# Kernel tuning notes

Measured on AMD Instinct MI355X. Metric: run time of the kernel, lower is better.

The kernel has to match this reference:

```python
import jax, jax.numpy as jnp
import numpy as np

N_NODES = 100000
N_EDGES = 1600000


def _lin_init(k, din, dout):
    # xavier-normal-ish weight, zero bias handled separately
    s = (2.0 / (din + dout)) ** 0.5
    return jax.random.normal(k, (din, dout), jnp.float32) * s


def setup_inputs() -> dict:
    key = jax.random.key(0)
    ks = jax.random.split(key, 32)
    inp = {
        "node_feat": jax.random.normal(ks[0], (N_NODES, 3), jnp.float32),
        "edge_feat": jax.random.normal(ks[1], (N_EDGES, 1), jnp.float32),
        "edge_dist": jax.random.normal(ks[2], (N_EDGES, 1), jnp.float32),
        "src": jax.random.randint(ks[3], (N_EDGES,), 0, N_NODES),
        "dst": jax.random.randint(ks[4], (N_EDGES,), 0, N_NODES),
    }
    dims = {"enc": [3, 64, 64, 8], "dec": [8, 64, 64, 1],
            "nod": [9, 64, 64, 8], "edg": [17, 64, 64, 1]}
    i = 5
    for name, d in dims.items():
        for l in range(3):
            inp[f"w_{name}{l+1}"] = _lin_init(ks[i], d[l], d[l + 1]); i += 1
            inp[f"b_{name}{l+1}"] = jnp.zeros((d[l + 1],), jnp.float32)
    return inp


def _mlp(x, w1, b1, w2, b2, w3, b3):
    x = jax.nn.relu(x @ w1 + b1)
    x = jax.nn.relu(x @ w2 + b2)
    return jax.nn.relu(x @ w3 + b3)


def _edge_softmax(dist, dst, n):
    # softmax over incoming edges per destination node (DGL edge_softmax)
    m = jax.ops.segment_max(dist, dst, num_segments=n)          # [N,1]
    e = jnp.exp(dist - m[dst])                                   # [E,1]
    s = jax.ops.segment_sum(e, dst, num_segments=n)              # [N,1]
    return e / s[dst]


def reference(node_feat, edge_feat, edge_dist, src, dst,
              w_enc1, b_enc1, w_enc2, b_enc2, w_enc3, b_enc3,
              w_dec1, b_dec1, w_dec2, b_dec2, w_dec3, b_dec3,
              w_nod1, b_nod1, w_nod2, b_nod2, w_nod3, b_nod3,
              w_edg1, b_edg1, w_edg2, b_edg2, w_edg3, b_edg3):
    n = node_feat.shape[0]
    # encoder: [N,3] -> [N,8]
    h = _mlp(node_feat, w_enc1, b_enc1, w_enc2, b_enc2, w_enc3, b_enc3)
    # softmax-weighted aggregation of src features to dst
    w = _edge_softmax(edge_dist, dst, n)                         # [E,1]
    h = jax.ops.segment_sum(w * h[src], dst, num_segments=n)     # [N,8]
    he = edge_feat                                               # [E,1]
    for _ in range(2):
        x = jnp.concatenate([he, h[src], h[dst]], axis=-1)       # [E,17]
        he = _mlp(x, w_edg1, b_edg1, w_edg2, b_edg2, w_edg3, b_edg3)  # [E,1]
        agg = jax.ops.segment_sum(he, dst, num_segments=n)       # [N,1]
        h = _mlp(jnp.concatenate([agg, h], axis=-1),
                 w_nod1, b_nod1, w_nod2, b_nod2, w_nod3, b_nod3)  # [N,8]
    # second softmax aggregation (same dist -> same weights)
    h = jax.ops.segment_sum(w * h[src], dst, num_segments=n)     # [N,8]
    # decoder: [N,8] -> [N,1]
    return _mlp(h, w_dec1, b_dec1, w_dec2, b_dec2, w_dec3, b_dec3)
```

## Files before the change

kernel.cpp:

```cpp
#include <hip/hip_runtime.h>
#include <hip/hip_bf16.h>

#define N_NODES 100000
#define N_EDGES 1600000

typedef __attribute__((ext_vector_type(4))) float f32x4;
typedef __attribute__((ext_vector_type(8))) short bf16x8;

__device__ __forceinline__ unsigned short f2bf(float v) {
    return __builtin_bit_cast(unsigned short, __float2bfloat16(v));
}
__device__ __forceinline__ float bf2f(unsigned short h) {
    return __uint_as_float(((unsigned)h) << 16);
}

__global__ void zero_kernel(float* p, int n) {
    int i = blockIdx.x * blockDim.x + threadIdx.x;
    int stride = gridDim.x * blockDim.x;
    for (; i < n; i += stride) p[i] = 0.f;
}

__global__ void exp_agg_kernel(const float* __restrict__ dist,
                               const int* __restrict__ src, const int* __restrict__ dst,
                               const float* __restrict__ h,
                               float* __restrict__ s, float* __restrict__ wbuf,
                               float* __restrict__ hagg, int E) {
    int t = blockIdx.x * blockDim.x + threadIdx.x;
    if (t >= E * 8) return;
    int e = t >> 3, c = t & 7;
    float v = expf(dist[e]);
    int d = dst[e];
    if (c == 0) {
        wbuf[e] = v;
        atomicAdd(s + d, v);
    }
    atomicAdd(hagg + d * 8 + c, v * h[src[e] * 8 + c]);
}

__global__ void agg2_kernel(const float* __restrict__ wbuf, const float* __restrict__ h,
                            const int* __restrict__ src, const int* __restrict__ dst,
                            float* __restrict__ out, int E) {
    int t = blockIdx.x * blockDim.x + threadIdx.x;
    if (t >= E * 8) return;
    int e = t >> 3, c = t & 7;
    float v = wbuf[e];
    atomicAdd(out + dst[e] * 8 + c, v * h[src[e] * 8 + c]);
}

__global__ void norm_kernel(float* __restrict__ hagg, const float* __restrict__ s,
                            float* __restrict__ rs, int N) {
    int d = blockIdx.x * blockDim.x + threadIdx.x;
    if (d >= N) return;
    float r = 1.f / s[d];
    rs[d] = r;
    float4 a = *(const float4*)(hagg + d * 8);
    float4 b = *(const float4*)(hagg + d * 8 + 4);
    a.x *= r; a.y *= r; a.z *= r; a.w *= r;
    b.x *= r; b.y *= r; b.z *= r; b.w *= r;
    *(float4*)(hagg + d * 8) = a;
    *(float4*)(hagg + d * 8 + 4) = b;
}

struct PackArgs { const float *w1, *b1, *w2; float* out; int din, stride; };

__global__ void pack_kernel(PackArgs a0, PackArgs a1, PackArgs a2) {
    PackArgs a = (blockIdx.x == 0) ? a0 : (blockIdx.x == 1) ? a1 : a2;
    int k = threadIdx.x;
    float* row = a.out + k * a.stride;
    for (int j = 0; j < 64; ++j) row[j] = a.w2[k * 64 + j];
    for (int j = 0; j < a.din; ++j) row[64 + j] = a.w1[j * 64 + k];
    row[64 + a.din] = a.b1[k];
}

__global__ void pack_edge_kernel(const float* __restrict__ w1, const float* __restrict__ w2,
                                 unsigned short* __restrict__ w1hi, unsigned short* __restrict__ w1lo,
                                 unsigned short* __restrict__ w2hi, unsigned short* __restrict__ w2lo) {
    int c = threadIdx.x;
    for (int j = 0; j < 32; ++j) {
        float v = (j < 17) ? w1[j * 64 + c] : 0.f;
        unsigned short hi = f2bf(v);
        w1hi[c * 32 + j] = hi;
        w1lo[c * 32 + j] = f2bf(v - bf2f(hi));
    }
    int mt = c >> 4, row = c & 15;
    for (int ch = 0; ch < 64; ++ch) {
        int ks = ch >> 5, r5 = ch & 31;
        int i = ((r5 >> 4) << 2) | (r5 & 3);
        int g = (r5 >> 2) & 3;
        int dstIdx = (((mt * 2 + ks) * 16 + row) * 4 + g) * 8 + i;
        float v = w2[ch * 64 + c];
        unsigned short hi = f2bf(v);
        w2hi[dstIdx] = hi;
        w2lo[dstIdx] = f2bf(v - bf2f(hi));
    }
}

template <int DIN, int DOUT, int STRIDE>
__device__ __forceinline__ void mlp_fused(
    const float* __restrict__ x, const float* __restrict__ wp,
    const float* __restrict__ b2,
    const float* __restrict__ w3, const float* __restrict__ b3,
    float* __restrict__ out) {
    float h2[64];
#pragma unroll
    for (int j = 0; j < 64; ++j) h2[j] = b2[j];
    for (int k = 0; k < 64; ++k) {
        const float* row = wp + k * STRIDE;
        float a = row[64 + DIN];
#pragma unroll
        for (int j = 0; j < DIN; ++j) a = fmaf(x[j], row[64 + j], a);
        a = fmaxf(a, 0.f);
#pragma unroll
        for (int j = 0; j < 64; ++j) h2[j] = fmaf(a, row[j], h2[j]);
    }
    float acc[DOUT];
#pragma unroll
    for (int o = 0; o < DOUT; ++o) acc[o] = b3[o];
#pragma unroll
    for (int j = 0; j < 64; ++j) {
        float r = fmaxf(h2[j], 0.f);
#pragma unroll
        for (int o = 0; o < DOUT; ++o) acc[o] = fmaf(r, w3[j * DOUT + o], acc[o]);
    }
#pragma unroll
    for (int o = 0; o < DOUT; ++o) out[o] = fmaxf(acc[o], 0.f);
}

template <int CA, int CB, int DOUT, int STRIDE>
__global__ __launch_bounds__(256, 3) void node_mlp_kernel(
    const float* __restrict__ xa, const float* __restrict__ xb,
    const float* __restrict__ rs,
    const float* __restrict__ wp, const float* __restrict__ b2,
    const float* __restrict__ w3, const float* __restrict__ b3,
    float* __restrict__ out, int n) {
    constexpr int DIN = CA + CB;
    int i = blockIdx.x * 256 + threadIdx.x;
    if (i >= n) return;
    float scale = rs ? rs[i] : 1.f;
    float x[DIN];
#pragma unroll
    for (int k = 0; k < CA; ++k) x[k] = xa[i * CA + k] * scale;
    if (CB == 8) {
        float4 v0 = *(const float4*)(xb + i * 8);
        float4 v1 = *(const float4*)(xb + i * 8 + 4);
        x[CA + 0] = v0.x; x[CA + 1] = v0.y; x[CA + 2] = v0.z; x[CA + 3] = v0.w;
        x[CA + 4] = v1.x; x[CA + 5] = v1.y; x[CA + 6] = v1.z; x[CA + 7] = v1.w;
    }
    float o[DOUT];
    mlp_fused<DIN, DOUT, STRIDE>(x, wp, b2, w3, b3, o);
#pragma unroll
    for (int k = 0; k < DOUT; ++k) out[i * DOUT + k] = o[k];
}

__global__ __launch_bounds__(128, 2) void edge_mlp_mfma_kernel(
    const float* __restrict__ he_in, const float* __restrict__ h,
    const int* __restrict__ src, const int* __restrict__ dst,
    const unsigned short* __restrict__ w1hi, const unsigned short* __restrict__ w1lo,
    const unsigned short* __restrict__ w2hi, const unsigned short* __restrict__ w2lo,
    const float* __restrict__ b1, const float* __restrict__ b2,
    const float* __restrict__ w3, const float* __restrict__ b3,
    float* __restrict__ he_out, float* __restrict__ agg) {
    __shared__ __align__(16) unsigned char smem[2 * 10240];
    const int lane = threadIdx.x & 63, wv = threadIdx.x >> 6;
    unsigned char* W = smem + wv * 10240;
    const int ebase = (blockIdx.x * 2 + wv) * 64;

    {
        int e = ebase + lane;
        float x[32];
        x[0] = he_in[e];
        int sr = src[e], dd = dst[e];
        float4 a0 = *(const float4*)(h + sr * 8);
        float4 a1 = *(const float4*)(h + sr * 8 + 4);
        float4 d0 = *(const float4*)(h + dd * 8);
        float4 d1 = *(const float4*)(h + dd * 8 + 4);
        x[1] = a0.x;  x[2] = a0.y;  x[3] = a0.z;  x[4] = a0.w;
        x[5] = a1.x;  x[6] = a1.y;  x[7] = a1.z;  x[8] = a1.w;
        x[9] = d0.x;  x[10] = d0.y; x[11] = d0.z; x[12] = d0.w;
        x[13] = d1.x; x[14] = d1.y; x[15] = d1.z; x[16] = d1.w;
#pragma unroll
        for (int j = 17; j < 32; ++j) x[j] = 0.f;
        unsigned uh[16], ul[16];
#pragma unroll
        for (int jj = 0; jj < 16; ++jj) {
            unsigned short h0 = f2bf(x[2 * jj]);
            unsigned short h1v = f2bf(x[2 * jj + 1]);
            unsigned short l0 = f2bf(x[2 * jj] - bf2f(h0));
            unsigned short l1 = f2bf(x[2 * jj + 1] - bf2f(h1v));
            uh[jj] = (unsigned)h0 | ((unsigned)h1v << 16);
            ul[jj] = (unsigned)l0 | ((unsigned)l1 << 16);
        }
        uint4* ph = (uint4*)(W + lane * 80);
        uint4* pl = (uint4*)(W + 5120 + lane * 80);
#pragma unroll
        for (int q = 0; q < 4; ++q) {
            ph[q] = make_uint4(uh[4 * q], uh[4 * q + 1], uh[4 * q + 2], uh[4 * q + 3]);
            pl[q] = make_uint4(ul[4 * q], ul[4 * q + 1], ul[4 * q + 2], ul[4 * q + 3]);
        }
    }
    __syncthreads();
    const int row = lane & 15, g = lane >> 4;

    bf16x8 wa_h[4], wa_l[4];
#pragma unroll
    for (int mt = 0; mt < 4; ++mt) {
        wa_h[mt] = *(const bf16x8*)(w1hi + (16 * mt + row) * 32 + g * 8);
        wa_l[mt] = *(const bf16x8*)(w1lo + (16 * mt + row) * 32 + g * 8);
    }
    bf16x8 xb_h[4], xb_l[4];
#pragma unroll
    for (int nt = 0; nt < 4; ++nt) {
        xb_h[nt] = *(const bf16x8*)(W + (16 * nt + row) * 80 + g * 16);
        xb_l[nt] = *(const bf16x8*)(W + 5120 + (16 * nt + row) * 80 + g * 16);
    }
    f32x4 c1[4][4];
#pragma unroll
    for (int mt = 0; mt < 4; ++mt)
#pragma unroll
        for (int nt = 0; nt < 4; ++nt) {
            f32x4 c = {0.f, 0.f, 0.f, 0.f};
            c = __builtin_amdgcn_mfma_f32_16x16x32_bf16(wa_h[mt], xb_h[nt], c, 0, 0, 0);
            c = __builtin_amdgcn_mfma_f32_16x16x32_bf16(wa_h[mt], xb_l[nt], c, 0, 0, 0);
            c = __builtin_amdgcn_mfma_f32_16x16x32_bf16(wa_l[mt], xb_h[nt], c, 0, 0, 0);
            c1[mt][nt] = c;
        }

    float4 b1v[4];
#pragma unroll
    for (int mt = 0; mt < 4; ++mt) b1v[mt] = *(const float4*)(b1 + 16 * mt + g * 4);
    bf16x8 pb_h[4][2], pb_l[4][2];
#pragma unroll
    for (int nt = 0; nt < 4; ++nt)
#pragma unroll
        for (int ks = 0; ks < 2; ++ks) {
            float v0 = fmaxf(c1[2 * ks][nt].x + b1v[2 * ks].x, 0.f);
            float v1 = fmaxf(c1[2 * ks][nt].y + b1v[2 * ks].y, 0.f);
            float v2 = fmaxf(c1[2 * ks][nt].z + b1v[2 * ks].z, 0.f);
            float v3 = fmaxf(c1[2 * ks][nt].w + b1v[2 * ks].w, 0.f);
            float v4 = fmaxf(c1[2 * ks + 1][nt].x + b1v[2 * ks + 1].x, 0.f);
            float v5 = fmaxf(c1[2 * ks + 1][nt].y + b1v[2 * ks + 1].y, 0.f);
            float v6 = fmaxf(c1[2 * ks + 1][nt].z + b1v[2 * ks + 1].z, 0.f);
            float v7 = fmaxf(c1[2 * ks + 1][nt].w + b1v[2 * ks + 1].w, 0.f);
            unsigned short h0 = f2bf(v0), h1v = f2bf(v1), h2v = f2bf(v2), h3 = f2bf(v3);
            unsigned short h4 = f2bf(v4), h5 = f2bf(v5), h6 = f2bf(v6), h7 = f2bf(v7);
            bf16x8 ph, pl;
            ph[0] = h0; ph[1] = h1v; ph[2] = h2v; ph[3] = h3;
            ph[4] = h4; ph[5] = h5;  ph[6] = h6;  ph[7] = h7;
            pl[0] = f2bf(v0 - bf2f(h0)); pl[1] = f2bf(v1 - bf2f(h1v));
            pl[2] = f2bf(v2 - bf2f(h2v)); pl[3] = f2bf(v3 - bf2f(h3));
            pl[4] = f2bf(v4 - bf2f(h4)); pl[5] = f2bf(v5 - bf2f(h5));
            pl[6] = f2bf(v6 - bf2f(h6)); pl[7] = f2bf(v7 - bf2f(h7));
            pb_h[nt][ks] = ph;
            pb_l[nt][ks] = pl;
        }

    f32x4 c2[4][4];
#pragma unroll
    for (int mt = 0; mt < 4; ++mt)
#pragma unroll
        for (int nt = 0; nt < 4; ++nt) c2[mt][nt] = (f32x4){0.f, 0.f, 0.f, 0.f};
#pragma unroll
    for (int mt = 0; mt < 4; ++mt) {
        bf16x8 w2a_h[2], w2a_l[2];
#pragma unroll
        for (int ks = 0; ks < 2; ++ks) {
            int off = (((mt * 2 + ks) * 16 + row) * 4 + g) * 8;
            w2a_h[ks] = *(const bf16x8*)(w2hi + off);
            w2a_l[ks] = *(const bf16x8*)(w2lo + off);
        }
#pragma unroll
        for (int nt = 0; nt < 4; ++nt)
#pragma unroll
            for (int ks = 0; ks < 2; ++ks) {
                c2[mt][nt] = __builtin_amdgcn_mfma_f32_16x16x32_bf16(w2a_h[ks], pb_h[nt][ks], c2[mt][nt], 0, 0, 0);
                c2[mt][nt] = __builtin_amdgcn_mfma_f32_16x16x32_bf16(w2a_h[ks], pb_l[nt][ks], c2[mt][nt], 0, 0, 0);
                c2[mt][nt] = __builtin_amdgcn_mfma_f32_16x16x32_bf16(w2a_l[ks], pb_h[nt][ks], c2[mt][nt], 0, 0, 0);
            }
    }

    float4 b2v[4], w3v[4];
#pragma unroll
    for (int mt = 0; mt < 4; ++mt) {
        b2v[mt] = *(const float4*)(b2 + 16 * mt + g * 4);
        w3v[mt] = *(const float4*)(w3 + 16 * mt + g * 4);
    }
    float b3s = b3[0];
    float pacc[4];
#pragma unroll
    for (int nt = 0; nt < 4; ++nt) {
        float p = 0.f;
#pragma unroll
        for (int mt = 0; mt < 4; ++mt) {
            p = fmaf(fmaxf(c2[mt][nt].x + b2v[mt].x, 0.f), w3v[mt].x, p);
            p = fmaf(fmaxf(c2[mt][nt].y + b2v[mt].y, 0.f), w3v[mt].y, p);
            p = fmaf(fmaxf(c2[mt][nt].z + b2v[mt].z, 0.f), w3v[mt].z, p);
            p = fmaf(fmaxf(c2[mt][nt].w + b2v[mt].w, 0.f), w3v[mt].w, p);
        }
        p += __shfl_xor(p, 16);
        p += __shfl_xor(p, 32);
        pacc[nt] = p;
    }
    if (lane < 16) {
#pragma unroll
        for (int nt = 0; nt < 4; ++nt) {
            int e2 = ebase + 16 * nt + lane;
            float o = fmaxf(pacc[nt] + b3s, 0.f);
            he_out[e2] = o;
            atomicAdd(agg + dst[e2], o);
        }
    }
}

extern "C" void kernel_launch(void* const* d_in, const int* in_sizes, int n_in,
                              void* d_out, int out_size, void* d_ws, size_t ws_size,
                              hipStream_t stream) {
    const int N = N_NODES, E = N_EDGES;
    const float* node_feat = (const float*)d_in[0];
    const float* edge_feat = (const float*)d_in[1];
    const float* edge_dist = (const float*)d_in[2];
    const int* src = (const int*)d_in[3];
    const int* dst = (const int*)d_in[4];
    const float* w_enc1 = (const float*)d_in[5];  const float* b_enc1 = (const float*)d_in[6];
    const float* w_enc2 = (const float*)d_in[7];  const float* b_enc2 = (const float*)d_in[8];
    const float* w_enc3 = (const float*)d_in[9];  const float* b_enc3 = (const float*)d_in[10];
    const float* w_dec1 = (const float*)d_in[11]; const float* b_dec1 = (const float*)d_in[12];
    const float* w_dec2 = (const float*)d_in[13]; const float* b_dec2 = (const float*)d_in[14];
    const float* w_dec3 = (const float*)d_in[15]; const float* b_dec3 = (const float*)d_in[16];
    const float* w_nod1 = (const float*)d_in[17]; const float* b_nod1 = (const float*)d_in[18];
    const float* w_nod2 = (const float*)d_in[19]; const float* b_nod2 = (const float*)d_in[20];
    const float* w_nod3 = (const float*)d_in[21]; const float* b_nod3 = (const float*)d_in[22];
    const float* w_edg1 = (const float*)d_in[23]; const float* b_edg1 = (const float*)d_in[24];
    const float* w_edg2 = (const float*)d_in[25]; const float* b_edg2 = (const float*)d_in[26];
    const float* w_edg3 = (const float*)d_in[27]; const float* b_edg3 = (const float*)d_in[28];

    float* ws = (float*)d_ws;
    float* s      = ws;
    float* hagg1  = ws + N;
    float* agg1   = ws + 9 * N;
    float* agg2   = ws + 10 * N;
    float* hagg2  = ws + 11 * N;
    float* rs     = ws + 19 * N;
    float* h_enc  = ws + 20 * N;
    float* h_r1   = ws + 28 * N;
    float* h_r2   = ws + 36 * N;
    float* wbuf   = ws + 44 * N;
    float* he1    = wbuf + E;
    float* he2    = he1 + E;
    float* pk_enc = he2 + E;
    float* pk_nod = pk_enc + 64 * 80;
    float* pk_dec = pk_nod + 64 * 80;
    unsigned short* w1hi = (unsigned short*)(pk_dec + 64 * 80);
    unsigned short* w1lo = w1hi + 64 * 32;
    unsigned short* w2hi = w1lo + 64 * 32;
    unsigned short* w2lo = w2hi + 64 * 64;

    PackArgs pa0{w_enc1, b_enc1, w_enc2, pk_enc, 3, 80};
    PackArgs pa1{w_nod1, b_nod1, w_nod2, pk_nod, 9, 80};
    PackArgs pa2{w_dec1, b_dec1, w_dec2, pk_dec, 8, 80};
    pack_kernel<<<3, 64, 0, stream>>>(pa0, pa1, pa2);
    pack_edge_kernel<<<1, 64, 0, stream>>>(w_edg1, w_edg2, w1hi, w1lo, w2hi, w2lo);

    zero_kernel<<<2048, 256, 0, stream>>>(ws, 19 * N);
    node_mlp_kernel<3, 0, 8, 80><<<(N + 255) / 256, 256, 0, stream>>>(node_feat, nullptr,
        nullptr, pk_enc, b_enc2, w_enc3, b_enc3, h_enc, N);
    exp_agg_kernel<<<(E * 8 + 255) / 256, 256, 0, stream>>>(edge_dist, src, dst, h_enc,
        s, wbuf, hagg1, E);
    norm_kernel<<<(N + 255) / 256, 256, 0, stream>>>(hagg1, s, rs, N);
    edge_mlp_mfma_kernel<<<E / 128, 128, 0, stream>>>(edge_feat, hagg1, src, dst,
        w1hi, w1lo, w2hi, w2lo, b_edg1, b_edg2, w_edg3, b_edg3, he1, agg1);
    node_mlp_kernel<1, 8, 8, 80><<<(N + 255) / 256, 256, 0, stream>>>(agg1, hagg1,
        nullptr, pk_nod, b_nod2, w_nod3, b_nod3, h_r1, N);
    edge_mlp_mfma_kernel<<<E / 128, 128, 0, stream>>>(he1, h_r1, src, dst,
        w1hi, w1lo, w2hi, w2lo, b_edg1, b_edg2, w_edg3, b_edg3, he2, agg2);
    node_mlp_kernel<1, 8, 8, 80><<<(N + 255) / 256, 256, 0, stream>>>(agg2, h_r1,
        nullptr, pk_nod, b_nod2, w_nod3, b_nod3, h_r2, N);
    agg2_kernel<<<(E * 8 + 255) / 256, 256, 0, stream>>>(wbuf, h_r2, src, dst, hagg2, E);
    node_mlp_kernel<8, 0, 1, 80><<<(N + 255) / 256, 256, 0, stream>>>(hagg2, nullptr,
        rs, pk_dec, b_dec2, w_dec3, b_dec3, (float*)d_out, N);
}
```

Before: 721.4 us.

## Stage raw fp32 edge inputs in LDS and process edge tiles one at a time

Result: slower. 802.6 us (+11.3%).

```diff
diff --git a/kernel.cpp b/kernel.cpp
--- a/kernel.cpp
+++ b/kernel.cpp
@@ -76,11 +76,11 @@
                                  unsigned short* __restrict__ w1hi, unsigned short* __restrict__ w1lo,
                                  unsigned short* __restrict__ w2hi, unsigned short* __restrict__ w2lo) {
     int c = threadIdx.x;
-    for (int j = 0; j < 32; ++j) {
-        float v = (j < 17) ? w1[j * 64 + c] : 0.f;
+    for (int k = 0; k < 32; ++k) {
+        float v = (k < 16) ? w1[(k + 1) * 64 + c] : (k == 16 ? w1[c] : 0.f);
         unsigned short hi = f2bf(v);
-        w1hi[c * 32 + j] = hi;
-        w1lo[c * 32 + j] = f2bf(v - bf2f(hi));
+        w1hi[c * 32 + k] = hi;
+        w1lo[c * 32 + k] = f2bf(v - bf2f(hi));
     }
     int mt = c >> 4, row = c & 15;
     for (int ch = 0; ch < 64; ++ch) {
@@ -152,7 +152,7 @@
     for (int k = 0; k < DOUT; ++k) out[i * DOUT + k] = o[k];
 }
 
-__global__ __launch_bounds__(128, 2) void edge_mlp_mfma_kernel(
+__global__ __launch_bounds__(128) void edge_mlp_mfma_kernel(
     const float* __restrict__ he_in, const float* __restrict__ h,
     const int* __restrict__ src, const int* __restrict__ dst,
     const unsigned short* __restrict__ w1hi, const unsigned short* __restrict__ w1lo,
@@ -160,43 +160,24 @@
     const float* __restrict__ b1, const float* __restrict__ b2,
     const float* __restrict__ w3, const float* __restrict__ b3,
     float* __restrict__ he_out, float* __restrict__ agg) {
-    __shared__ __align__(16) unsigned char smem[2 * 10240];
+    __shared__ __align__(16) float Xs[2][64][20];
     const int lane = threadIdx.x & 63, wv = threadIdx.x >> 6;
-    unsigned char* W = smem + wv * 10240;
+    float (*W)[20] = Xs[wv];
     const int ebase = (blockIdx.x * 2 + wv) * 64;
 
     {
         int e = ebase + lane;
-        float x[32];
-        x[0] = he_in[e];
         int sr = src[e], dd = dst[e];
-        float4 a0 = *(const float4*)(h + sr * 8);
-        float4 a1 = *(const float4*)(h + sr * 8 + 4);
-        float4 d0 = *(const float4*)(h + dd * 8);
-        float4 d1 = *(const float4*)(h + dd * 8 + 4);
-        x[1] = a0.x;  x[2] = a0.y;  x[3] = a0.z;  x[4] = a0.w;
-        x[5] = a1.x;  x[6] = a1.y;  x[7] = a1.z;  x[8] = a1.w;
-        x[9] = d0.x;  x[10] = d0.y; x[11] = d0.z; x[12] = d0.w;
-        x[13] = d1.x; x[14] = d1.y; x[15] = d1.z; x[16] = d1.w;
-#pragma unroll
-        for (int j = 17; j < 32; ++j) x[j] = 0.f;
-        unsigned uh[16], ul[16];
-#pragma unroll
-        for (int jj = 0; jj < 16; ++jj) {
-            unsigned short h0 = f2bf(x[2 * jj]);
-            unsigned short h1v = f2bf(x[2 * jj + 1]);
-            unsigned short l0 = f2bf(x[2 * jj] - bf2f(h0));
-            unsigned short l1 = f2bf(x[2 * jj + 1] - bf2f(h1v));
-            uh[jj] = (unsigned)h0 | ((unsigned)h1v << 16);
-            ul[jj] = (unsigned)l0 | ((unsigned)l1 << 16);
-        }
-        uint4* ph = (uint4*)(W + lane * 80);
-        uint4* pl = (uint4*)(W + 5120 + lane * 80);
-#pragma unroll
-        for (int q = 0; q < 4; ++q) {
-            ph[q] = make_uint4(uh[4 * q], uh[4 * q + 1], uh[4 * q + 2], uh[4 * q + 3]);
-            pl[q] = make_uint4(ul[4 * q], ul[4 * q + 1], ul[4 * q + 2], ul[4 * q + 3]);
-        }
+        float4 A0 = *(const float4*)(h + sr * 8);
+        float4 A1 = *(const float4*)(h + sr * 8 + 4);
+        float4 D0 = *(const float4*)(h + dd * 8);
+        float4 D1 = *(const float4*)(h + dd * 8 + 4);
+        float hev = he_in[e];
+        *(float4*)&W[lane][0]  = A0;
+        *(float4*)&W[lane][4]  = A1;
+        *(float4*)&W[lane][8]  = D0;
+        *(float4*)&W[lane][12] = D1;
+        W[lane][16] = hev;
     }
     __syncthreads();
     const int row = lane & 15, g = lane >> 4;
@@ -207,40 +188,58 @@
         wa_h[mt] = *(const bf16x8*)(w1hi + (16 * mt + row) * 32 + g * 8);
         wa_l[mt] = *(const bf16x8*)(w1lo + (16 * mt + row) * 32 + g * 8);
     }
-    bf16x8 xb_h[4], xb_l[4];
+    bf16x8 w2a_h[4][2];
+#pragma unroll
+    for (int mt = 0; mt < 4; ++mt)
+#pragma unroll
+        for (int ks = 0; ks < 2; ++ks)
+            w2a_h[mt][ks] = *(const bf16x8*)(w2hi + (((mt * 2 + ks) * 16 + row) * 4 + g) * 8);
+    float4 b1v[4];
+#pragma unroll
+    for (int mt = 0; mt < 4; ++mt) b1v[mt] = *(const float4*)(b1 + 16 * mt + g * 4);
+    float b3s = b3[0];
+
+    float pacc[4];
 #pragma unroll
     for (int nt = 0; nt < 4; ++nt) {
-        xb_h[nt] = *(const bf16x8*)(W + (16 * nt + row) * 80 + g * 16);
-        xb_l[nt] = *(const bf16x8*)(W + 5120 + (16 * nt + row) * 80 + g * 16);
-    }
-    f32x4 c1[4][4];
-#pragma unroll
-    for (int mt = 0; mt < 4; ++mt)
-#pragma unroll
-        for (int nt = 0; nt < 4; ++nt) {
+        bf16x8 xh = {}, xl = {};
+        if (g < 2) {
+            const float* xr = &W[16 * nt + row][g * 8];
+            float4 u = *(const float4*)xr;
+            float4 v = *(const float4*)(xr + 4);
+            float vals[8] = {u.x, u.y, u.z, u.w, v.x, v.y, v.z, v.w};
+#pragma unroll
+            for (int j = 0; j < 8; ++j) {
+                unsigned short hb = f2bf(vals[j]);
+                xh[j] = (short)hb;
+                xl[j] = (short)f2bf(vals[j] - bf2f(hb));
+            }
+        } else if (g == 2) {
+            float hv = W[16 * nt + row][16];
+            unsigned short hb = f2bf(hv);
+            xh[0] = (short)hb;
+            xl[0] = (short)f2bf(hv - bf2f(hb));
+        }
+        f32x4 c1[4];
+#pragma unroll
+        for (int mt = 0; mt < 4; ++mt) {
             f32x4 c = {0.f, 0.f, 0.f, 0.f};
-            c = __builtin_amdgcn_mfma_f32_16x16x32_bf16(wa_h[mt], xb_h[nt], c, 0, 0, 0);
-            c = __builtin_amdgcn_mfma_f32_16x16x32_bf16(wa_h[mt], xb_l[nt], c, 0, 0, 0);
-            c = __builtin_amdgcn_mfma_f32_16x16x32_bf16(wa_l[mt], xb_h[nt], c, 0, 0, 0);
-            c1[mt][nt] = c;
-        }
-
-    float4 b1v[4];
-#pragma unroll
-    for (int mt = 0; mt < 4; ++mt) b1v[mt] = *(const float4*)(b1 + 16 * mt + g * 4);
-    bf16x8 pb_h[4][2], pb_l[4][2];
-#pragma unroll
-    for (int nt = 0; nt < 4; ++nt)
+            c = __builtin_amdgcn_mfma_f32_16x16x32_bf16(wa_h[mt], xh, c, 0, 0, 0);
+            c = __builtin_amdgcn_mfma_f32_16x16x32_bf16(wa_h[mt], xl, c, 0, 0, 0);
+            c = __builtin_amdgcn_mfma_f32_16x16x32_bf16(wa_l[mt], xh, c, 0, 0, 0);
+            c1[mt] = c;
+        }
+        bf16x8 pb_h[2], pb_l[2];
 #pragma unroll
         for (int ks = 0; ks < 2; ++ks) {
-            float v0 = fmaxf(c1[2 * ks][nt].x + b1v[2 * ks].x, 0.f);
-            float v1 = fmaxf(c1[2 * ks][nt].y + b1v[2 * ks].y, 0.f);
-            float v2 = fmaxf(c1[2 * ks][nt].z + b1v[2 * ks].z, 0.f);
-            float v3 = fmaxf(c1[2 * ks][nt].w + b1v[2 * ks].w, 0.f);
-            float v4 = fmaxf(c1[2 * ks + 1][nt].x + b1v[2 * ks + 1].x, 0.f);
-            float v5 = fmaxf(c1[2 * ks + 1][nt].y + b1v[2 * ks + 1].y, 0.f);
-            float v6 = fmaxf(c1[2 * ks + 1][nt].z + b1v[2 * ks + 1].z, 0.f);
-            float v7 = fmaxf(c1[2 * ks + 1][nt].w + b1v[2 * ks + 1].w, 0.f);
+            float v0 = fmaxf(c1[2 * ks].x + b1v[2 * ks].x, 0.f);
+            float v1 = fmaxf(c1[2 * ks].y + b1v[2 * ks].y, 0.f);
+            float v2 = fmaxf(c1[2 * ks].z + b1v[2 * ks].z, 0.f);
+            float v3 = fmaxf(c1[2 * ks].w + b1v[2 * ks].w, 0.f);
+            float v4 = fmaxf(c1[2 * ks + 1].x + b1v[2 * ks + 1].x, 0.f);
+            float v5 = fmaxf(c1[2 * ks + 1].y + b1v[2 * ks + 1].y, 0.f);
+            float v6 = fmaxf(c1[2 * ks + 1].z + b1v[2 * ks + 1].z, 0.f);
+            float v7 = fmaxf(c1[2 * ks + 1].w + b1v[2 * ks + 1].w, 0.f);
             unsigned short h0 = f2bf(v0), h1v = f2bf(v1), h2v = f2bf(v2), h3 = f2bf(v3);
             unsigned short h4 = f2bf(v4), h5 = f2bf(v5), h6 = f2bf(v6), h7 = f2bf(v7);
             bf16x8 ph, pl;
@@ -250,51 +249,31 @@
             pl[2] = f2bf(v2 - bf2f(h2v)); pl[3] = f2bf(v3 - bf2f(h3));
             pl[4] = f2bf(v4 - bf2f(h4)); pl[5] = f2bf(v5 - bf2f(h5));
             pl[6] = f2bf(v6 - bf2f(h6)); pl[7] = f2bf(v7 - bf2f(h7));
-            pb_h[nt][ks] = ph;
-            pb_l[nt][ks] = pl;
-        }
-
-    f32x4 c2[4][4];
-#pragma unroll
-    for (int mt = 0; mt < 4; ++mt)
-#pragma unroll
-        for (int nt = 0; nt < 4; ++nt) c2[mt][nt] = (f32x4){0.f, 0.f, 0.f, 0.f};
-#pragma unroll
-    for (int mt = 0; mt < 4; ++mt) {
-        bf16x8 w2a_h[2], w2a_l[2];
-#pragma unroll
-        for (int ks = 0; ks < 2; ++ks) {
-            int off = (((mt * 2 + ks) * 16 + row) * 4 + g) * 8;
-            w2a_h[ks] = *(const bf16x8*)(w2hi + off);
-            w2a_l[ks] = *(const bf16x8*)(w2lo + off);
-        }
-#pragma unroll
-        for (int nt = 0; nt < 4; ++nt)
+            pb_h[ks] = ph;
+            pb_l[ks] = pl;
+        }
+        f32x4 c2[4];
+#pragma unroll
+        for (int mt = 0; mt < 4; ++mt) {
+            f32x4 c = {0.f, 0.f, 0.f, 0.f};
 #pragma unroll
             for (int ks = 0; ks < 2; ++ks) {
-                c2[mt][nt] = __builtin_amdgcn_mfma_f32_16x16x32_bf16(w2a_h[ks], pb_h[nt][ks], c2[mt][nt], 0, 0, 0);
-                c2[mt][nt] = __builtin_amdgcn_mfma_f32_16x16x32_bf16(w2a_h[ks], pb_l[nt][ks], c2[mt][nt], 0, 0, 0);
-                c2[mt][nt] = __builtin_amdgcn_mfma_f32_16x16x32_bf16(w2a_l[ks], pb_h[nt][ks], c2[mt][nt], 0, 0, 0);
+                bf16x8 wl = *(const bf16x8*)(w2lo + (((mt * 2 + ks) * 16 + row) * 4 + g) * 8);
+                c = __builtin_amdgcn_mfma_f32_16x16x32_bf16(w2a_h[mt][ks], pb_h[ks], c, 0, 0, 0);
+                c = __builtin_amdgcn_mfma_f32_16x16x32_bf16(w2a_h[mt][ks], pb_l[ks], c, 0, 0, 0);
+                c = __builtin_amdgcn_mfma_f32_16x16x32_bf16(wl, pb_h[ks], c, 0, 0, 0);
             }
-    }
-
-    float4 b2v[4], w3v[4];
-#pragma unroll
-    for (int mt = 0; mt < 4; ++mt) {
-        b2v[mt] = *(const float4*)(b2 + 16 * mt + g * 4);
-        w3v[mt] = *(const float4*)(w3 + 16 * mt + g * 4);
-    }
-    float b3s = b3[0];
-    float pacc[4];
-#pragma unroll
-    for (int nt = 0; nt < 4; ++nt) {
+            c2[mt] = c;
+        }
         float p = 0.f;
 #pragma unroll
         for (int mt = 0; mt < 4; ++mt) {
-            p = fmaf(fmaxf(c2[mt][nt].x + b2v[mt].x, 0.f), w3v[mt].x, p);
-            p = fmaf(fmaxf(c2[mt][nt].y + b2v[mt].y, 0.f), w3v[mt].y, p);
-            p = fmaf(fmaxf(c2[mt][nt].z + b2v[mt].z, 0.f), w3v[mt].z, p);
-            p = fmaf(fmaxf(c2[mt][nt].w + b2v[mt].w, 0.f), w3v[mt].w, p);
+            float4 bb = *(const float4*)(b2 + 16 * mt + g * 4);
+            float4 ww = *(const float4*)(w3 + 16 * mt + g * 4);
+            p = fmaf(fmaxf(c2[mt].x + bb.x, 0.f), ww.x, p);
+            p = fmaf(fmaxf(c2[mt].y + bb.y, 0.f), ww.y, p);
+            p = fmaf(fmaxf(c2[mt].z + bb.z, 0.f), ww.z, p);
+            p = fmaf(fmaxf(c2[mt].w + bb.w, 0.f), ww.w, p);
         }
         p += __shfl_xor(p, 16);
         p += __shfl_xor(p, 32);
```
